# Performance work log

Hardware: AMD Instinct MI355X
Metric: run time of the kernel (lower is better)

Reference implementation:

```python
import jax, jax.numpy as jnp
import numpy as np

N = 200000
D_STRUCT = 131
D_SPATIAL = 64
D_OUT = 256


def setup_inputs() -> dict:
    key = jax.random.key(0)
    k1, k2, k3, k4, k5, k6, k7 = jax.random.split(key, 7)
    spatial = jax.random.normal(k1, (N, D_SPATIAL), dtype=jnp.float32)
    structural = jax.random.normal(k2, (N, D_STRUCT), dtype=jnp.float32)
    neighbour = jax.random.randint(k3, (N, 3), 0, N, dtype=jnp.int64)
    # Conv1d(kernel=1) params: weight [out_ch, in_ch], bias [out_ch]
    fan_agg = D_STRUCT
    W_agg = jax.random.uniform(k4, (D_OUT, D_STRUCT), dtype=jnp.float32,
                               minval=-1.0, maxval=1.0) / np.sqrt(fan_agg)
    b_agg = jax.random.uniform(k5, (D_OUT,), dtype=jnp.float32,
                               minval=-1.0, maxval=1.0) / np.sqrt(fan_agg)
    fan_comb = D_SPATIAL + D_STRUCT
    W_comb = jax.random.uniform(k6, (D_OUT, D_SPATIAL + D_STRUCT), dtype=jnp.float32,
                                minval=-1.0, maxval=1.0) / np.sqrt(fan_comb)
    b_comb = jax.random.uniform(k7, (D_OUT,), dtype=jnp.float32,
                                minval=-1.0, maxval=1.0) / np.sqrt(fan_comb)
    return {"spatial": spatial, "structural": structural, "neighbour": neighbour,
            "W_agg": W_agg, "b_agg": b_agg, "W_comb": W_comb, "b_comb": b_comb}


def reference(spatial, structural, neighbour, W_agg, b_agg, W_comb, b_comb):
    # Combination1: concat(spatial, structural) -> 1x1 conv (linear)
    a1 = jnp.concatenate([spatial, structural], axis=1)  # [n, 195]
    out1 = a1 @ W_comb.T + b_comb                         # [n, 256]

    # Aggregation1: mean of self + 3 gathered neighbour rows, then linear
    neigh_feats = structural[neighbour]                   # [n, 3, 131]
    agg = (structural + neigh_feats.sum(axis=1)) * 0.25   # [n, 131]
    out2 = agg @ W_agg.T + b_agg                          # [n, 256]
    return (out1, out2)
```

## Files before the change

### kernel.cpp

```cpp
#include <hip/hip_runtime.h>
#include <hip/hip_bf16.h>

#define NROWS   200000
#define DSP     64
#define DST     131
#define DOUT    256
#define K1PAD   224
#define K2PAD   160
#define NK1     7
#define NK2     5
#define BM      64
#define NBLK    (NROWS / BM)
#define LD1     (K1PAD + 8)
#define LD2     (K2PAD + 8)

typedef short bf8   __attribute__((ext_vector_type(8)));
typedef float f32x4 __attribute__((ext_vector_type(4)));

__device__ __forceinline__ unsigned short f2bf(float x) {
    unsigned u = __float_as_uint(x);
    unsigned r = (u + 0x7fffu + ((u >> 16) & 1u)) >> 16;
    return (unsigned short)r;
}
__device__ __forceinline__ unsigned pack2(unsigned short lo, unsigned short hi) {
    return (unsigned)lo | ((unsigned)hi << 16);
}

__global__ __launch_bounds__(256) void wprep(const float* __restrict__ Wc,
                                             const float* __restrict__ Wa,
                                             short* __restrict__ w1p,
                                             short* __restrict__ w2p) {
    int idx = blockIdx.x * 256 + threadIdx.x;
    if (idx < 57344) {
        int j  = idx & 7;
        int l  = (idx >> 3) & 63;
        int cb = (idx >> 9) & 15;
        int ks = idx >> 13;
        int k  = ks * 32 + (l >> 4) * 8 + j;
        int n  = cb * 16 + (l & 15);
        float v = (k < 195) ? Wc[n * 195 + k] : 0.0f;
        w1p[idx] = (short)f2bf(v);
    } else {
        int id2 = idx - 57344;
        if (id2 < 40960) {
            int j  = id2 & 7;
            int l  = (id2 >> 3) & 63;
            int cb = (id2 >> 9) & 15;
            int ks = id2 >> 13;
            int k  = ks * 32 + (l >> 4) * 8 + j;
            int n  = cb * 16 + (l & 15);
            float v = (k < 131) ? Wa[n * 131 + k] : 0.0f;
            w2p[id2] = (short)f2bf(v);
        }
    }
}

template <int NK, int LDPAD>
__device__ __forceinline__ void mfma_tile_and_store(
        const short (*lds)[LDPAD],
        const short* __restrict__ wp,
        const float* __restrict__ bias,
        float* __restrict__ out,
        int r0, int t) {
    const int wave = t >> 6;
    const int l    = t & 63;
    const int lr   = l & 15;
    const int lk   = l >> 4;

    f32x4 acc[4][4];
    #pragma unroll
    for (int m = 0; m < 4; ++m)
        #pragma unroll
        for (int n = 0; n < 4; ++n)
            acc[m][n] = (f32x4){0.f, 0.f, 0.f, 0.f};

    #pragma unroll
    for (int ks = 0; ks < NK; ++ks) {
        bf8 a[4], bb[4];
        #pragma unroll
        for (int m = 0; m < 4; ++m)
            a[m] = *(const bf8*)&lds[m * 16 + lr][ks * 32 + lk * 8];
        #pragma unroll
        for (int n = 0; n < 4; ++n) {
            int cb = wave * 4 + n;
            bb[n] = *(const bf8*)(wp + (((ks * 16 + cb) * 64 + l) << 3));
        }
        #pragma unroll
        for (int m = 0; m < 4; ++m)
            #pragma unroll
            for (int n = 0; n < 4; ++n)
                acc[m][n] = __builtin_amdgcn_mfma_f32_16x16x32_bf16(
                                a[m], bb[n], acc[m][n], 0, 0, 0);
    }

    #pragma unroll
    for (int n = 0; n < 4; ++n) {
        int col = wave * 64 + n * 16 + lr;
        float bv = bias[col];
        #pragma unroll
        for (int m = 0; m < 4; ++m) {
            #pragma unroll
            for (int r = 0; r < 4; ++r) {
                int row = m * 16 + lk * 4 + r;
                out[(size_t)(r0 + row) * DOUT + col] = acc[m][n][r] + bv;
            }
        }
    }
}

__global__ __launch_bounds__(256) void fused(const float* __restrict__ spatial,
                                             const float* __restrict__ structural,
                                             const int*   __restrict__ neigh,
                                             const short* __restrict__ w1p,
                                             const short* __restrict__ w2p,
                                             const float* __restrict__ b_comb,
                                             const float* __restrict__ b_agg,
                                             float* __restrict__ out1,
                                             float* __restrict__ out2) {
    __shared__ short lds1[BM][LD1];
    __shared__ short lds2[BM][LD2];
    const int t  = threadIdx.x;
    const int r0 = blockIdx.x * BM;

    {
        int row = t >> 2;
        int j   = t & 3;
        for (int c = 195 + j; c < K1PAD; c += 4) lds1[row][c] = 0;
        for (int c = 131 + j; c < K2PAD; c += 4) lds2[row][c] = 0;
    }

    {
        int h  = t & 15;
        int sl = t >> 4;
        #pragma unroll
        for (int p = 0; p < 4; ++p) {
            int row = sl + 16 * p;
            float4 v = *(const float4*)(spatial + (size_t)(r0 + row) * DSP + 4 * h);
            uint2 w;
            w.x = pack2(f2bf(v.x), f2bf(v.y));
            w.y = pack2(f2bf(v.z), f2bf(v.w));
            *(uint2*)&lds1[row][4 * h] = w;
        }
    }

    {
        int g = t & 31;
        int s = t >> 5;
        #pragma unroll
        for (int p = 0; p < 8; ++p) {
            int rr = s + 8 * p;
            size_t r = (size_t)(r0 + rr);
            const float* s0 = structural + r * DST;
            const int*   nb = neigh + r * 3;
            int n0 = nb[0], n1 = nb[1], n2 = nb[2];
            const float* p1 = structural + (size_t)n0 * DST;
            const float* p2 = structural + (size_t)n1 * DST;
            const float* p3 = structural + (size_t)n2 * DST;
            #pragma unroll
            for (int i = 0; i < 4; ++i) {
                int c = g + 32 * i;
                float v0 = s0[c];
                float a  = v0 + p1[c] + p2[c] + p3[c];
                lds1[rr][DSP + c] = (short)f2bf(v0);
                lds2[rr][c]       = (short)f2bf(a * 0.25f);
            }
            if (g < 3) {
                int c = 128 + g;
                float v0 = s0[c];
                float a  = v0 + p1[c] + p2[c] + p3[c];
                lds1[rr][DSP + c] = (short)f2bf(v0);
                lds2[rr][c]       = (short)f2bf(a * 0.25f);
            }
        }
    }
    __syncthreads();

    mfma_tile_and_store<NK1, LD1>(lds1, w1p, b_comb, out1, r0, t);
    mfma_tile_and_store<NK2, LD2>(lds2, w2p, b_agg, out2, r0, t);
}

extern "C" void kernel_launch(void* const* d_in, const int* in_sizes, int n_in,
                              void* d_out, int out_size, void* d_ws, size_t ws_size,
                              hipStream_t stream) {
    const float* spatial    = (const float*)d_in[0];
    const float* structural = (const float*)d_in[1];
    const int*   neighbour  = (const int*)  d_in[2];
    const float* W_agg      = (const float*)d_in[3];
    const float* b_agg      = (const float*)d_in[4];
    const float* W_comb     = (const float*)d_in[5];
    const float* b_comb     = (const float*)d_in[6];

    float* out1 = (float*)d_out;
    float* out2 = out1 + (size_t)NROWS * DOUT;

    short* w1p = (short*)d_ws;
    short* w2p = w1p + 57344;

    wprep<<<384, 256, 0, stream>>>(W_comb, W_agg, w1p, w2p);
    fused<<<NBLK, 256, 0, stream>>>(spatial, structural, neighbour,
                                    w1p, w2p, b_comb, b_agg, out1, out2);
}
```

Before: 211.6 us.

## Halve row tile to 32 and restructure gather to one wave per row

Shrinks the per-block row tile from 64 to 32, templating the MFMA tile over the number of 16-row repeats, and adds an occupancy hint of 6 blocks per SM. The structural gather is reorganised so each wave handles 8 whole rows with 64 lanes reading contiguous columns, and the zero padding is folded into the gather instead of a separate pass. This aims to raise occupancy and improve coalescing of the gather, at the cost of fewer MFMAs per weight-fragment load from global memory, so weights are re-read twice as often.

```diff
diff --git a/kernel.cpp b/kernel.cpp
--- a/kernel.cpp
+++ b/kernel.cpp
@@ -9,7 +9,7 @@
 #define K2PAD   160
 #define NK1     7
 #define NK2     5
-#define BM      64
+#define BM      32
 #define NBLK    (NROWS / BM)
 #define LD1     (K1PAD + 8)
 #define LD2     (K2PAD + 8)
@@ -55,7 +55,7 @@
     }
 }
 
-template <int NK, int LDPAD>
+template <int NK, int LDPAD, int MREP>
 __device__ __forceinline__ void mfma_tile_and_store(
         const short (*lds)[LDPAD],
         const short* __restrict__ wp,
@@ -67,18 +67,18 @@
     const int lr   = l & 15;
     const int lk   = l >> 4;
 
-    f32x4 acc[4][4];
+    f32x4 acc[MREP][4];
     #pragma unroll
-    for (int m = 0; m < 4; ++m)
+    for (int m = 0; m < MREP; ++m)
         #pragma unroll
         for (int n = 0; n < 4; ++n)
             acc[m][n] = (f32x4){0.f, 0.f, 0.f, 0.f};
 
     #pragma unroll
     for (int ks = 0; ks < NK; ++ks) {
-        bf8 a[4], bb[4];
-        #pragma unroll
-        for (int m = 0; m < 4; ++m)
+        bf8 a[MREP], bb[4];
+        #pragma unroll
+        for (int m = 0; m < MREP; ++m)
             a[m] = *(const bf8*)&lds[m * 16 + lr][ks * 32 + lk * 8];
         #pragma unroll
         for (int n = 0; n < 4; ++n) {
@@ -86,7 +86,7 @@
             bb[n] = *(const bf8*)(wp + (((ks * 16 + cb) * 64 + l) << 3));
         }
         #pragma unroll
-        for (int m = 0; m < 4; ++m)
+        for (int m = 0; m < MREP; ++m)
             #pragma unroll
             for (int n = 0; n < 4; ++n)
                 acc[m][n] = __builtin_amdgcn_mfma_f32_16x16x32_bf16(
@@ -98,7 +98,7 @@
         int col = wave * 64 + n * 16 + lr;
         float bv = bias[col];
         #pragma unroll
-        for (int m = 0; m < 4; ++m) {
+        for (int m = 0; m < MREP; ++m) {
             #pragma unroll
             for (int r = 0; r < 4; ++r) {
                 int row = m * 16 + lk * 4 + r;
@@ -108,32 +108,28 @@
     }
 }
 
-__global__ __launch_bounds__(256) void fused(const float* __restrict__ spatial,
-                                             const float* __restrict__ structural,
-                                             const int*   __restrict__ neigh,
-                                             const short* __restrict__ w1p,
-                                             const short* __restrict__ w2p,
-                                             const float* __restrict__ b_comb,
-                                             const float* __restrict__ b_agg,
-                                             float* __restrict__ out1,
-                                             float* __restrict__ out2) {
+__global__ __launch_bounds__(256, 6) void fused(
+        const float* __restrict__ spatial,
+        const float* __restrict__ structural,
+        const int*   __restrict__ neigh,
+        const short* __restrict__ w1p,
+        const short* __restrict__ w2p,
+        const float* __restrict__ b_comb,
+        const float* __restrict__ b_agg,
+        float* __restrict__ out1,
+        float* __restrict__ out2) {
     __shared__ short lds1[BM][LD1];
     __shared__ short lds2[BM][LD2];
-    const int t  = threadIdx.x;
-    const int r0 = blockIdx.x * BM;
-
-    {
-        int row = t >> 2;
-        int j   = t & 3;
-        for (int c = 195 + j; c < K1PAD; c += 4) lds1[row][c] = 0;
-        for (int c = 131 + j; c < K2PAD; c += 4) lds2[row][c] = 0;
-    }
+    const int t    = threadIdx.x;
+    const int wave = t >> 6;
+    const int l    = t & 63;
+    const int r0   = blockIdx.x * BM;
 
     {
         int h  = t & 15;
         int sl = t >> 4;
         #pragma unroll
-        for (int p = 0; p < 4; ++p) {
+        for (int p = 0; p < 2; ++p) {
             int row = sl + 16 * p;
             float4 v = *(const float4*)(spatial + (size_t)(r0 + row) * DSP + 4 * h);
             uint2 w;
@@ -144,39 +140,41 @@
     }
 
     {
-        int g = t & 31;
-        int s = t >> 5;
-        #pragma unroll
-        for (int p = 0; p < 8; ++p) {
-            int rr = s + 8 * p;
-            size_t r = (size_t)(r0 + rr);
+        const int rowb = wave * 8;
+        #pragma unroll 4
+        for (int rr = 0; rr < 8; ++rr) {
+            int row = rowb + rr;
+            size_t r = (size_t)(r0 + row);
             const float* s0 = structural + r * DST;
-            const int*   nb = neigh + r * 3;
-            int n0 = nb[0], n1 = nb[1], n2 = nb[2];
+            int n0 = neigh[r * 3 + 0];
+            int n1 = neigh[r * 3 + 1];
+            int n2 = neigh[r * 3 + 2];
             const float* p1 = structural + (size_t)n0 * DST;
             const float* p2 = structural + (size_t)n1 * DST;
             const float* p3 = structural + (size_t)n2 * DST;
-            #pragma unroll
-            for (int i = 0; i < 4; ++i) {
-                int c = g + 32 * i;
-                float v0 = s0[c];
-                float a  = v0 + p1[c] + p2[c] + p3[c];
-                lds1[rr][DSP + c] = (short)f2bf(v0);
-                lds2[rr][c]       = (short)f2bf(a * 0.25f);
+
+            float a0 = s0[l],      b0 = p1[l],      c0 = p2[l],      d0 = p3[l];
+            float a1 = s0[l + 64], b1 = p1[l + 64], c1 = p2[l + 64], d1 = p3[l + 64];
+            lds1[row][64 + l]  = (short)f2bf(a0);
+            lds1[row][128 + l] = (short)f2bf(a1);
+            lds2[row][l]       = (short)f2bf((a0 + b0 + c0 + d0) * 0.25f);
+            lds2[row][64 + l]  = (short)f2bf((a1 + b1 + c1 + d1) * 0.25f);
+
+            if (l < 3) {
+                float a2 = s0[128 + l], b2 = p1[128 + l],
+                      c2 = p2[128 + l], d2 = p3[128 + l];
+                lds1[row][192 + l] = (short)f2bf(a2);
+                lds2[row][128 + l] = (short)f2bf((a2 + b2 + c2 + d2) * 0.25f);
+            } else if (l < 32) {
+                lds1[row][192 + l] = 0;
+                lds2[row][128 + l] = 0;
             }
-            if (g < 3) {
-                int c = 128 + g;
-                float v0 = s0[c];
-                float a  = v0 + p1[c] + p2[c] + p3[c];
-                lds1[rr][DSP + c] = (short)f2bf(v0);
-                lds2[rr][c]       = (short)f2bf(a * 0.25f);
-            }
         }
     }
     __syncthreads();
 
-    mfma_tile_and_store<NK1, LD1>(lds1, w1p, b_comb, out1, r0, t);
-    mfma_tile_and_store<NK2, LD2>(lds2, w2p, b_agg, out2, r0, t);
+    mfma_tile_and_store<NK1, LD1, BM / 16>(lds1, w1p, b_comb, out1, r0, t);
+    mfma_tile_and_store<NK2, LD2, BM / 16>(lds2, w2p, b_agg, out2, r0, t);
 }
 
 extern "C" void kernel_launch(void* const* d_in, const int* in_sizes, int n_in,
```

After: 275.5 us. 30.2% more time.

## Pre-convert structural to padded bf16 and gather MFMA operands directly from global

Applied to the files above, without the earlier changes.

Adds a pre-pass kernel that converts the structural matrix into a bf16 copy whose rows are padded to 136 elements. The main kernel then reads its MFMA A-fragments straight from global memory (spatial in fp32 converted on the fly, structural in bf16) instead of staging them in LDS. The neighbour gather reads this half-size bf16 copy, and the mean is summed in fp32 from the bf16 values. The goal is to cut the bytes of the random gathers, drop the LDS staging and its barrier, and raise occupancy. The cost is an extra conversion pass and workspace traffic, plus a small precision change from rounding to bf16 before the sum.

```diff
diff --git a/kernel.cpp b/kernel.cpp
--- a/kernel.cpp
+++ b/kernel.cpp
@@ -4,15 +4,10 @@
 #define NROWS   200000
 #define DSP     64
 #define DST     131
+#define DSTP    136
 #define DOUT    256
-#define K1PAD   224
-#define K2PAD   160
-#define NK1     7
-#define NK2     5
 #define BM      64
 #define NBLK    (NROWS / BM)
-#define LD1     (K1PAD + 8)
-#define LD2     (K2PAD + 8)
 
 typedef short bf8   __attribute__((ext_vector_type(8)));
 typedef float f32x4 __attribute__((ext_vector_type(4)));
@@ -22,8 +17,38 @@
     unsigned r = (u + 0x7fffu + ((u >> 16) & 1u)) >> 16;
     return (unsigned short)r;
 }
-__device__ __forceinline__ unsigned pack2(unsigned short lo, unsigned short hi) {
-    return (unsigned)lo | ((unsigned)hi << 16);
+__device__ __forceinline__ unsigned short bf1(float x) {
+    __hip_bfloat16 h = __float2bfloat16(x);
+    return *reinterpret_cast<unsigned short*>(&h);
+}
+__device__ __forceinline__ unsigned packbf2(float a, float b) {
+    return (unsigned)bf1(a) | ((unsigned)bf1(b) << 16);
+}
+__device__ __forceinline__ float blo(unsigned u) { return __uint_as_float(u << 16); }
+__device__ __forceinline__ float bhi(unsigned u) { return __uint_as_float(u & 0xffff0000u); }
+
+union bf8u { bf8 b; uint4 u; };
+
+__device__ __forceinline__ bf8 mk8(float4 u, float4 v) {
+    bf8u r;
+    r.u.x = packbf2(u.x, u.y);
+    r.u.y = packbf2(u.z, u.w);
+    r.u.z = packbf2(v.x, v.y);
+    r.u.w = packbf2(v.z, v.w);
+    return r.b;
+}
+
+__device__ __forceinline__ bf8 aggsum(bf8 s0, bf8 s1, bf8 s2, bf8 s3) {
+    bf8u a{s0}, b{s1}, c{s2}, d{s3}, r;
+    #pragma unroll
+    for (int i = 0; i < 4; ++i) {
+        unsigned ua = (&a.u.x)[i], ub = (&b.u.x)[i];
+        unsigned uc = (&c.u.x)[i], ud = (&d.u.x)[i];
+        float lo = (blo(ua) + blo(ub)) + (blo(uc) + blo(ud));
+        float hi = (bhi(ua) + bhi(ub)) + (bhi(uc) + bhi(ud));
+        (&r.u.x)[i] = packbf2(lo * 0.25f, hi * 0.25f);
+    }
+    return r.b;
 }
 
 __global__ __launch_bounds__(256) void wprep(const float* __restrict__ Wc,
@@ -55,17 +80,58 @@
     }
 }
 
-template <int NK, int LDPAD>
-__device__ __forceinline__ void mfma_tile_and_store(
-        const short (*lds)[LDPAD],
-        const short* __restrict__ wp,
-        const float* __restrict__ bias,
-        float* __restrict__ out,
-        int r0, int t) {
-    const int wave = t >> 6;
-    const int l    = t & 63;
-    const int lr   = l & 15;
-    const int lk   = l >> 4;
+__global__ __launch_bounds__(256) void cvt(const float* __restrict__ st,
+                                           unsigned short* __restrict__ sbf) {
+    int wid = (blockIdx.x * 256 + threadIdx.x) >> 6;
+    int l   = threadIdx.x & 63;
+    int h   = l >> 5, sub = l & 31;
+    int nw  = (gridDim.x * 256) >> 6;
+    for (int pr = wid; pr < NROWS / 2; pr += nw) {
+        int row = pr * 2 + h;
+        const float* src = st + (size_t)row * DST;
+        unsigned short* dst = sbf + (size_t)row * DSTP;
+        float4 v = *(const float4*)(src + 4 * sub);
+        uint2 wv;
+        wv.x = packbf2(v.x, v.y);
+        wv.y = packbf2(v.z, v.w);
+        *(uint2*)(dst + 4 * sub) = wv;
+        if (sub == 0) {
+            float4 tl = *(const float4*)(src + 127);
+            uint4 tw;
+            tw.x = packbf2(tl.y, tl.z);
+            tw.y = packbf2(tl.w, 0.0f);
+            tw.z = 0u;
+            tw.w = 0u;
+            *(uint4*)(dst + 128) = tw;
+        }
+    }
+}
+
+__global__ __launch_bounds__(256, 3) void mesh_gemm(
+        const float* __restrict__ spatial,
+        const unsigned short* __restrict__ sbf,
+        const int*   __restrict__ neigh,
+        const short* __restrict__ w1p,
+        const short* __restrict__ w2p,
+        const float* __restrict__ b_comb,
+        const float* __restrict__ b_agg,
+        float* __restrict__ out1,
+        float* __restrict__ out2) {
+    const int t  = threadIdx.x;
+    const int w  = t >> 6;
+    const int l  = t & 63;
+    const int lr = l & 15;
+    const int lk = l >> 4;
+    const int r0 = blockIdx.x * BM;
+
+    const float*          sp[4];
+    const unsigned short* ss[4];
+    #pragma unroll
+    for (int m = 0; m < 4; ++m) {
+        int row = r0 + m * 16 + lr;
+        sp[m] = spatial + (size_t)row * DSP;
+        ss[m] = sbf + (size_t)row * DSTP;
+    }
 
     f32x4 acc[4][4];
     #pragma unroll
@@ -75,108 +141,122 @@
             acc[m][n] = (f32x4){0.f, 0.f, 0.f, 0.f};
 
     #pragma unroll
-    for (int ks = 0; ks < NK; ++ks) {
-        bf8 a[4], bb[4];
+    for (int ks = 0; ks < 7; ++ks) {
+        bf8 a[4];
+        if (ks < 2) {
+            #pragma unroll
+            for (int m = 0; m < 4; ++m) {
+                const float* p = sp[m] + ks * 32 + lk * 8;
+                float4 u = *(const float4*)(p);
+                float4 v = *(const float4*)(p + 4);
+                a[m] = mk8(u, v);
+            }
+        } else if (ks < 6) {
+            #pragma unroll
+            for (int m = 0; m < 4; ++m)
+                a[m] = *(const bf8*)(ss[m] + (ks - 2) * 32 + lk * 8);
+        } else {
+            #pragma unroll
+            for (int m = 0; m < 4; ++m) {
+                bf8 z = {};
+                if (lk == 0) z = *(const bf8*)(ss[m] + 128);
+                a[m] = z;
+            }
+        }
+        #pragma unroll
+        for (int n = 0; n < 4; ++n) {
+            int cb = w * 4 + n;
+            bf8 b = *(const bf8*)(w1p + (((ks * 16 + cb) * 64 + l) << 3));
+            #pragma unroll
+            for (int m = 0; m < 4; ++m)
+                acc[m][n] = __builtin_amdgcn_mfma_f32_16x16x32_bf16(
+                                a[m], b, acc[m][n], 0, 0, 0);
+        }
+    }
+    #pragma unroll
+    for (int n = 0; n < 4; ++n) {
+        int col = w * 64 + n * 16 + lr;
+        float bv = b_comb[col];
         #pragma unroll
         for (int m = 0; m < 4; ++m)
-            a[m] = *(const bf8*)&lds[m * 16 + lr][ks * 32 + lk * 8];
+            #pragma unroll
+            for (int r = 0; r < 4; ++r)
+                out1[(size_t)(r0 + m * 16 + lk * 4 + r) * DOUT + col]
+                    = acc[m][n][r] + bv;
+    }
+
+    const int rb = (r0 + l) * 3;
+    int nq0 = neigh[rb + 0];
+    int nq1 = neigh[rb + 1];
+    int nq2 = neigh[rb + 2];
+
+    const unsigned short* np[4][3];
+    #pragma unroll
+    for (int m = 0; m < 4; ++m) {
+        int src = m * 16 + lr;
+        int i0 = __shfl(nq0, src);
+        int i1 = __shfl(nq1, src);
+        int i2 = __shfl(nq2, src);
+        np[m][0] = sbf + (size_t)i0 * DSTP;
+        np[m][1] = sbf + (size_t)i1 * DSTP;
+        np[m][2] = sbf + (size_t)i2 * DSTP;
+    }
+
+    f32x4 acc2[4][4];
+    #pragma unroll
+    for (int m = 0; m < 4; ++m)
+        #pragma unroll
+        for (int n = 0; n < 4; ++n)
+            acc2[m][n] = (f32x4){0.f, 0.f, 0.f, 0.f};
+
+    #pragma unroll
+    for (int ks = 0; ks < 5; ++ks) {
+        bf8 a[4];
+        if (ks < 4) {
+            int off = ks * 32 + lk * 8;
+            #pragma unroll
+            for (int m = 0; m < 4; ++m) {
+                bf8 s0 = *(const bf8*)(ss[m]    + off);
+                bf8 s1 = *(const bf8*)(np[m][0] + off);
+                bf8 s2 = *(const bf8*)(np[m][1] + off);
+                bf8 s3 = *(const bf8*)(np[m][2] + off);
+                a[m] = aggsum(s0, s1, s2, s3);
+            }
+        } else {
+            #pragma unroll
+            for (int m = 0; m < 4; ++m) {
+                bf8 z = {};
+                if (lk == 0) {
+                    bf8 s0 = *(const bf8*)(ss[m]    + 128);
+                    bf8 s1 = *(const bf8*)(np[m][0] + 128);
+                    bf8 s2 = *(const bf8*)(np[m][1] + 128);
+                    bf8 s3 = *(const bf8*)(np[m][2] + 128);
+                    z = aggsum(s0, s1, s2, s3);
+                }
+                a[m] = z;
+            }
+        }
         #pragma unroll
         for (int n = 0; n < 4; ++n) {
-            int cb = wave * 4 + n;
-            bb[n] = *(const bf8*)(wp + (((ks * 16 + cb) * 64 + l) << 3));
-        }
+            int cb = w * 4 + n;
+            bf8 b = *(const bf8*)(w2p + (((ks * 16 + cb) * 64 + l) << 3));
+            #pragma unroll
+            for (int m = 0; m < 4; ++m)
+                acc2[m][n] = __builtin_amdgcn_mfma_f32_16x16x32_bf16(
+                                a[m], b, acc2[m][n], 0, 0, 0);
+        }
+    }
+    #pragma unroll
+    for (int n = 0; n < 4; ++n) {
+        int col = w * 64 + n * 16 + lr;
+        float bv = b_agg[col];
         #pragma unroll
         for (int m = 0; m < 4; ++m)
             #pragma unroll
-            for (int n = 0; n < 4; ++n)
-                acc[m][n] = __builtin_amdgcn_mfma_f32_16x16x32_bf16(
-                                a[m], bb[n], acc[m][n], 0, 0, 0);
-    }
-
-    #pragma unroll
-    for (int n = 0; n < 4; ++n) {
-        int col = wave * 64 + n * 16 + lr;
-        float bv = bias[col];
-        #pragma unroll
-        for (int m = 0; m < 4; ++m) {
-            #pragma unroll
-            for (int r = 0; r < 4; ++r) {
-                int row = m * 16 + lk * 4 + r;
-                out[(size_t)(r0 + row) * DOUT + col] = acc[m][n][r] + bv;
-            }
-        }
-    }
-}
-
-__global__ __launch_bounds__(256) void fused(const float* __restrict__ spatial,
-                                             const float* __restrict__ structural,
-                                             const int*   __restrict__ neigh,
-                                             const short* __restrict__ w1p,
-                                             const short* __restrict__ w2p,
-                                             const float* __restrict__ b_comb,
-                                             const float* __restrict__ b_agg,
-                                             float* __restrict__ out1,
-                                             float* __restrict__ out2) {
-    __shared__ short lds1[BM][LD1];
-    __shared__ short lds2[BM][LD2];
-    const int t  = threadIdx.x;
-    const int r0 = blockIdx.x * BM;
-
-    {
-        int row = t >> 2;
-        int j   = t & 3;
-        for (int c = 195 + j; c < K1PAD; c += 4) lds1[row][c] = 0;
-        for (int c = 131 + j; c < K2PAD; c += 4) lds2[row][c] = 0;
-    }
-
-    {
-        int h  = t & 15;
-        int sl = t >> 4;
-        #pragma unroll
-        for (int p = 0; p < 4; ++p) {
-            int row = sl + 16 * p;
-            float4 v = *(const float4*)(spatial + (size_t)(r0 + row) * DSP + 4 * h);
-            uint2 w;
-            w.x = pack2(f2bf(v.x), f2bf(v.y));
-            w.y = pack2(f2bf(v.z), f2bf(v.w));
-            *(uint2*)&lds1[row][4 * h] = w;
-        }
-    }
-
-    {
-        int g = t & 31;
-        int s = t >> 5;
-        #pragma unroll
-        for (int p = 0; p < 8; ++p) {
-            int rr = s + 8 * p;
-            size_t r = (size_t)(r0 + rr);
-            const float* s0 = structural + r * DST;
-            const int*   nb = neigh + r * 3;
-            int n0 = nb[0], n1 = nb[1], n2 = nb[2];
-            const float* p1 = structural + (size_t)n0 * DST;
-            const float* p2 = structural + (size_t)n1 * DST;
-            const float* p3 = structural + (size_t)n2 * DST;
-            #pragma unroll
-            for (int i = 0; i < 4; ++i) {
-                int c = g + 32 * i;
-                float v0 = s0[c];
-                float a  = v0 + p1[c] + p2[c] + p3[c];
-                lds1[rr][DSP + c] = (short)f2bf(v0);
-                lds2[rr][c]       = (short)f2bf(a * 0.25f);
-            }
-            if (g < 3) {
-                int c = 128 + g;
-                float v0 = s0[c];
-                float a  = v0 + p1[c] + p2[c] + p3[c];
-                lds1[rr][DSP + c] = (short)f2bf(v0);
-                lds2[rr][c]       = (short)f2bf(a * 0.25f);
-            }
-        }
-    }
-    __syncthreads();
-
-    mfma_tile_and_store<NK1, LD1>(lds1, w1p, b_comb, out1, r0, t);
-    mfma_tile_and_store<NK2, LD2>(lds2, w2p, b_agg, out2, r0, t);
+            for (int r = 0; r < 4; ++r)
+                out2[(size_t)(r0 + m * 16 + lk * 4 + r) * DOUT + col]
+                    = acc2[m][n][r] + bv;
+    }
 }
 
 extern "C" void kernel_launch(void* const* d_in, const int* in_sizes, int n_in,
@@ -195,8 +275,10 @@
 
     short* w1p = (short*)d_ws;
     short* w2p = w1p + 57344;
+    unsigned short* sbf = (unsigned short*)((char*)d_ws + 196608);
 
     wprep<<<384, 256, 0, stream>>>(W_comb, W_agg, w1p, w2p);
-    fused<<<NBLK, 256, 0, stream>>>(spatial, structural, neighbour,
-                                    w1p, w2p, b_comb, b_agg, out1, out2);
-}
+    cvt<<<2048, 256, 0, stream>>>(structural, sbf);
+    mesh_gemm<<<NBLK, 256, 0, stream>>>(spatial, sbf, neighbour,
+                                        w1p, w2p, b_comb, b_agg, out1, out2);
+}
```

Result: slower. 324.0 us (+53.1%).
